# Optimization experiments

Measured on AMD Instinct MI355X. Metric: run time of the kernel, lower is better.

Reference implementation:

```python
import jax, jax.numpy as jnp
import numpy as np

G, K, C, H, D, L = 256, 88, 256, 8, 32, 4
NID, GATE, HID, ACT, NW = 16, 128, 256, 4644, 1
N = G * K
DEG = 16
E_RAND = N * DEG


def setup_inputs() -> dict:
    key = jax.random.key(0)
    ks = jax.random.split(key, 32)
    x = jax.random.normal(ks[0], (N, NID), dtype=jnp.float32)
    # within-graph random edges + self loops (PyG GATv2 add_self_loops=True)
    goff = jnp.repeat(jnp.arange(G, dtype=jnp.int64), K * DEG) * K
    src = goff + jax.random.randint(ks[1], (E_RAND,), 0, K, dtype=jnp.int64)
    dst = goff + jax.random.randint(ks[2], (E_RAND,), 0, K, dtype=jnp.int64)
    loops = jnp.arange(N, dtype=jnp.int64)
    edge_index = jnp.stack([jnp.concatenate([src, loops]), jnp.concatenate([dst, loops])])
    batch_map = jnp.repeat(jnp.arange(G, dtype=jnp.int64), K)

    def lin(k, fi, fo):
        return jax.random.normal(k, (fi, fo), dtype=jnp.float32) / np.sqrt(fi)

    inp = dict(x=x, edge_index=edge_index, batch_map=batch_map, num_graphs=G)
    inp['W_emb'] = lin(ks[3], NID, C); inp['b_emb'] = jnp.zeros((C,), jnp.float32)
    inp['pos_emb'] = jax.random.normal(ks[4], (K, C), dtype=jnp.float32)
    inp['gat_Wsrc'] = jax.random.normal(ks[5], (L, C, C), dtype=jnp.float32) / np.sqrt(C)
    inp['gat_Wdst'] = jax.random.normal(ks[6], (L, C, C), dtype=jnp.float32) / np.sqrt(C)
    inp['gat_att'] = jax.random.normal(ks[7], (L, H, D), dtype=jnp.float32) / np.sqrt(D)
    inp['gat_bias'] = jnp.zeros((L, C), jnp.float32)
    inp['ln_g'] = jnp.ones((L, C), jnp.float32); inp['ln_b'] = jnp.zeros((L, C), jnp.float32)
    inp['gW1'] = lin(ks[8], C, GATE); inp['gb1'] = jnp.zeros((GATE,), jnp.float32)
    inp['gW2'] = lin(ks[9], GATE, 1); inp['gb2'] = jnp.zeros((1,), jnp.float32)
    inp['pW1'] = lin(ks[10], C, HID); inp['pb1'] = jnp.zeros((HID,), jnp.float32)
    inp['p_ln_g'] = jnp.ones((HID,), jnp.float32); inp['p_ln_b'] = jnp.zeros((HID,), jnp.float32)
    inp['pW2'] = lin(ks[11], HID, ACT); inp['pb2'] = jnp.zeros((ACT,), jnp.float32)
    inp['vW1'] = lin(ks[12], C, HID); inp['vb1'] = jnp.zeros((HID,), jnp.float32)
    inp['vW2'] = lin(ks[13], HID, NW); inp['vb2'] = jnp.zeros((NW,), jnp.float32)
    return inp


def _layernorm(h, g, b):
    mu = h.mean(-1, keepdims=True)
    var = h.var(-1, keepdims=True)
    return (h - mu) * jax.lax.rsqrt(var + 1e-5) * g + b


def _segment_softmax(e, seg, num):
    m = jax.ops.segment_max(e, seg, num_segments=num)
    a = jnp.exp(e - m[seg])
    d = jax.ops.segment_sum(a, seg, num_segments=num)
    return a / d[seg]


def reference(x, edge_index, batch_map, num_graphs, W_emb, b_emb, pos_emb,
              gat_Wsrc, gat_Wdst, gat_att, gat_bias, ln_g, ln_b,
              gW1, gb1, gW2, gb2, pW1, pb1, p_ln_g, p_ln_b, pW2, pb2,
              vW1, vb1, vW2, vb2):
    n = x.shape[0]
    src, dst = edge_index[0], edge_index[1]
    h = jax.nn.relu(x @ W_emb + b_emb)
    positions = jnp.arange(n) % pos_emb.shape[0]  # arange(K) repeated per graph
    h = h + pos_emb[positions]
    for l in range(gat_Wsrc.shape[0]):
        xl = (h @ gat_Wsrc[l]).reshape(n, H, D)  # source transform
        xr = (h @ gat_Wdst[l]).reshape(n, H, D)  # target transform
        z = jax.nn.leaky_relu(xl[src] + xr[dst], negative_slope=0.2)  # [E,H,D]
        e = jnp.einsum('ehd,hd->eh', z, gat_att[l])
        alpha = _segment_softmax(e, dst, n)  # softmax over incoming edges
        out = jax.ops.segment_sum(alpha[:, :, None] * xl[src], dst, num_segments=n)
        out = out.reshape(n, -1) + gat_bias[l]
        h = _layernorm(h + jax.nn.relu(out), ln_g[l], ln_b[l])
    # gated attentional pooling over graphs
    gate = (jax.nn.relu(h @ gW1 + gb1) @ gW2 + gb2)[:, 0]
    a = _segment_softmax(gate, batch_map, num_graphs)
    emb = jax.ops.segment_sum(a[:, None] * h, batch_map, num_segments=num_graphs)
    policy = jax.nn.relu(_layernorm(emb @ pW1 + pb1, p_ln_g, p_ln_b)) @ pW2 + pb2
    value = jnp.tanh(jax.nn.relu(emb @ vW1 + vb1) @ vW2 + vb2)
    return policy, value
```

## Files before the change

### kernel.cpp

```cpp
#include <hip/hip_runtime.h>
#include <math.h>

constexpr int CN = 256;
constexpr int NHEAD = 8;
constexpr int KPG = 88;
constexpr int NIDF = 16;
constexpr int GATE_DIM = 128;
constexpr int ACT_DIM = 4644;
constexpr float LOG2E = 1.4426950408889634f;

typedef __attribute__((ext_vector_type(8))) short bf16x8;
typedef __attribute__((ext_vector_type(4))) float f32x4;

__device__ __forceinline__ unsigned short f2bf(float f) {
    unsigned int u = __float_as_uint(f);
    unsigned int r = (u + 0x7fffu + ((u >> 16) & 1u)) >> 16;
    return (unsigned short)r;
}
__device__ __forceinline__ float bf2f(unsigned short h) {
    return __uint_as_float(((unsigned int)h) << 16);
}

__device__ __forceinline__ void glds16(const void* g, void* l) {
    __builtin_amdgcn_global_load_lds(
        (const __attribute__((address_space(1))) unsigned int*)g,
        (__attribute__((address_space(3))) unsigned int*)l, 16, 0, 0);
}

__device__ __forceinline__ float fexp2(float x) {
    float r;
    asm("v_exp_f32 %0, %1" : "=v"(r) : "v"(x));
    return r;
}

__device__ __forceinline__ float grp8_sum(float p) {
    int t;
    t = __builtin_amdgcn_mov_dpp(__float_as_int(p), 0xB1, 0xF, 0xF, true);
    p += __int_as_float(t);
    t = __builtin_amdgcn_mov_dpp(__float_as_int(p), 0x4E, 0xF, 0xF, true);
    p += __int_as_float(t);
    t = __builtin_amdgcn_mov_dpp(__float_as_int(p), 0x141, 0xF, 0xF, true);
    p += __int_as_float(t);
    return p;
}

__global__ void count_kernel(const int* __restrict__ dst, int* __restrict__ cnt, int E) {
    int e = blockIdx.x * 256 + threadIdx.x;
    if (e < E) atomicAdd(&cnt[dst[e]], 1);
}

__global__ __launch_bounds__(1024) void scan1_kernel(const int* __restrict__ cnt,
                                                     int* __restrict__ rowptr,
                                                     int* __restrict__ btot, int n) {
    __shared__ int buf[1024];
    int tid = threadIdx.x;
    int i = blockIdx.x * 1024 + tid;
    int v = (i < n) ? cnt[i] : 0;
    buf[tid] = v;
    __syncthreads();
    for (int off = 1; off < 1024; off <<= 1) {
        int t = (tid >= off) ? buf[tid - off] : 0;
        __syncthreads();
        buf[tid] += t;
        __syncthreads();
    }
    if (i < n) rowptr[i] = buf[tid] - v;
    if (tid == 1023) btot[blockIdx.x] = buf[1023];
}

__global__ void scan2_kernel(int* __restrict__ btot, int nb) {
    if (threadIdx.x == 0 && blockIdx.x == 0) {
        int s = 0;
        for (int b = 0; b < nb; ++b) { int t = btot[b]; btot[b] = s; s += t; }
        btot[nb] = s;
    }
}

__global__ __launch_bounds__(1024) void scan3_kernel(int* __restrict__ rowptr,
                                                     const int* __restrict__ btot,
                                                     int n, int nb) {
    int i = blockIdx.x * 1024 + threadIdx.x;
    if (i < n) rowptr[i] += btot[i >> 10];
    else if (i == n) rowptr[n] = btot[nb];
}

__global__ void fill_kernel(const int* __restrict__ src, const int* __restrict__ dst,
                            const int* __restrict__ rowptr, int* __restrict__ cursor,
                            int* __restrict__ csrcB, int E) {
    int e = blockIdx.x * 256 + threadIdx.x;
    if (e < E) {
        int d = dst[e];
        int p = atomicAdd(&cursor[d], 1);
        csrcB[rowptr[d] + p] = src[e] * 1024;
    }
}

__global__ __launch_bounds__(256) void embed_kernel(const float* __restrict__ x,
                                                    const float* __restrict__ Wemb,
                                                    const float* __restrict__ bemb,
                                                    const float* __restrict__ pos,
                                                    float* __restrict__ h,
                                                    unsigned short* __restrict__ hh) {
    __shared__ float Wl[NIDF][CN];
    int tid = threadIdx.x;
    for (int i = tid; i < NIDF * CN; i += 256) Wl[i >> 8][i & 255] = Wemb[i];
    __syncthreads();
    float bias = bemb[tid];
    int node0 = blockIdx.x * 16;
    for (int q = 0; q < 16; ++q) {
        int n = node0 + q;
        float acc = bias;
        #pragma unroll
        for (int k = 0; k < NIDF; ++k) acc += x[n * NIDF + k] * Wl[k][tid];
        float val = fmaxf(acc, 0.f) + pos[(n % KPG) * CN + tid];
        h[(size_t)n * CN + tid] = val;
        hh[(size_t)n * CN + tid] = f2bf(val);
    }
}

__global__ void wconv_cat_kernel(const float* __restrict__ Ws, const float* __restrict__ Wd,
                                 unsigned short* __restrict__ Bh,
                                 unsigned short* __restrict__ Bl, int NB, int tot) {
    int o = blockIdx.x * 256 + threadIdx.x;
    if (o >= tot) return;
    int l4 = blockIdx.y;
    const float* ws = Ws + (size_t)l4 * 256 * 256;
    const float* wd = Wd + (size_t)l4 * 256 * 256;
    int idx = o & 511;
    int nb = (o >> 9) % NB;
    int kb = o / (512 * NB);
    int l = idx >> 3, j = idx & 7;
    int k = kb * 32 + (l >> 4) * 8 + j;
    int c = nb * 16 + (l & 15);
    float v = (c < 256) ? ws[(size_t)k * 256 + c] : wd[(size_t)k * 256 + (c - 256)];
    unsigned short hh = f2bf(v);
    Bh[(size_t)l4 * tot + o] = hh;
    Bl[(size_t)l4 * tot + o] = f2bf(v - bf2f(hh));
}

__global__ void wconv_kernel(const float* __restrict__ W, unsigned short* __restrict__ Bh,
                             unsigned short* __restrict__ Bl, int Nn, int NB, int tot) {
    int o = blockIdx.x * 256 + threadIdx.x;
    if (o >= tot) return;
    int idx = o & 511;
    int nb = (o >> 9) % NB;
    int kb = o / (512 * NB);
    int l = idx >> 3, j = idx & 7;
    int k = kb * 32 + (l >> 4) * 8 + j;
    int c = nb * 16 + (l & 15);
    float v = (c < Nn) ? W[(size_t)k * Nn + c] : 0.f;
    unsigned short hh = f2bf(v);
    Bh[o] = hh;
    Bl[o] = f2bf(v - bf2f(hh));
}

template <bool BIAS, bool THREE, bool OBF16, int NBT>
__global__ __launch_bounds__(256) void mgemm(const unsigned short* __restrict__ Ah,
                                             const unsigned short* __restrict__ Al,
                                             const unsigned short* __restrict__ Bh,
                                             const unsigned short* __restrict__ Bl,
                                             const float* __restrict__ bias,
                                             void* __restrict__ Cv,
                                             int M, int Nlog, int NB, int K) {
    constexpr int NF = NBT / 2;
    __shared__ unsigned short AhL[8 * 64 * 8];
    __shared__ unsigned short AlL[THREE ? 8 * 64 * 8 : 16];
    __shared__ unsigned short BhL[NBT * 512];
    __shared__ unsigned short BlL[NBT * 512];
    int tid = threadIdx.x;
    int wid = tid >> 6, lane = tid & 63;
    int row0 = blockIdx.x * 128;
    int cb = blockIdx.y;
    int wr = wid >> 1, wc = wid & 1;

    int rr = lane & 15, kq = lane >> 4;

    f32x4 acc[4][NF] = {};

    for (int k0 = 0; k0 < K; k0 += 32) {
        int kb = k0 >> 5;
        {
            int mb0 = wid * 2;
            const unsigned short* s0 = Ah + (size_t)(row0 + mb0 * 16 + rr) * K + k0 + kq * 8;
            const unsigned short* s1 = Ah + (size_t)(row0 + mb0 * 16 + 16 + rr) * K + k0 + kq * 8;
            glds16(s0, &AhL[mb0 * 512]);
            glds16(s1, &AhL[mb0 * 512 + 512]);
            if constexpr (THREE) {
                const unsigned short* t0 = Al + (size_t)(row0 + mb0 * 16 + rr) * K + k0 + kq * 8;
                const unsigned short* t1 = Al + (size_t)(row0 + mb0 * 16 + 16 + rr) * K + k0 + kq * 8;
                glds16(t0, &AlL[mb0 * 512]);
                glds16(t1, &AlL[mb0 * 512 + 512]);
            }
        }
        {
            size_t base = ((size_t)kb * NB + (size_t)cb * NBT) * 512;
            for (int ch = wid; ch < NBT; ch += 4) {
                glds16(Bh + base + ch * 512 + lane * 8, &BhL[ch * 512]);
                glds16(Bl + base + ch * 512 + lane * 8, &BlL[ch * 512]);
            }
        }
        __syncthreads();
        bf16x8 a_h[4], a_l[4], b_h[NF], b_l[NF];
        #pragma unroll
        for (int mf = 0; mf < 4; ++mf) {
            int off = ((wr * 4 + mf) * 64 + lane) * 8;
            a_h[mf] = *reinterpret_cast<const bf16x8*>(&AhL[off]);
            if constexpr (THREE)
                a_l[mf] = *reinterpret_cast<const bf16x8*>(&AlL[off]);
        }
        #pragma unroll
        for (int nf = 0; nf < NF; ++nf) {
            int off = ((wc * NF + nf) * 64 + lane) * 8;
            b_h[nf] = *reinterpret_cast<const bf16x8*>(&BhL[off]);
            b_l[nf] = *reinterpret_cast<const bf16x8*>(&BlL[off]);
        }
        #pragma unroll
        for (int mf = 0; mf < 4; ++mf)
            #pragma unroll
            for (int nf = 0; nf < NF; ++nf) {
                acc[mf][nf] = __builtin_amdgcn_mfma_f32_16x16x32_bf16(a_h[mf], b_h[nf], acc[mf][nf], 0, 0, 0);
                acc[mf][nf] = __builtin_amdgcn_mfma_f32_16x16x32_bf16(a_h[mf], b_l[nf], acc[mf][nf], 0, 0, 0);
                if constexpr (THREE)
                    acc[mf][nf] = __builtin_amdgcn_mfma_f32_16x16x32_bf16(a_l[mf], b_h[nf], acc[mf][nf], 0, 0, 0);
            }
        __syncthreads();
    }
    #pragma unroll
    for (int mf = 0; mf < 4; ++mf) {
        #pragma unroll
        for (int nf = 0; nf < NF; ++nf) {
            int col = cb * (NBT * 16) + wc * (NF * 16) + nf * 16 + (lane & 15);
            if (col < Nlog) {
                float bv = BIAS ? bias[col] : 0.f;
                #pragma unroll
                for (int rg = 0; rg < 4; ++rg) {
                    int row = row0 + wr * 64 + mf * 16 + (lane >> 4) * 4 + rg;
                    float r = acc[mf][nf][rg] + bv;
                    if constexpr (OBF16)
                        ((unsigned short*)Cv)[(size_t)row * Nlog + col] = f2bf(r);
                    else
                        ((float*)Cv)[(size_t)row * Nlog + col] = r;
                }
            }
        }
    }
}

__global__ __launch_bounds__(64) void gat_agg(const unsigned short* __restrict__ xlr,
                                              const int* __restrict__ rowptr,
                                              const int* __restrict__ csrcB,
                                              const float* __restrict__ att,
                                              const float* __restrict__ bias,
                                              const float* __restrict__ lng,
                                              const float* __restrict__ lnb,
                                              float* __restrict__ h,
                                              unsigned short* __restrict__ hh) {
    int cpx = gridDim.x >> 3;
    int swz = (blockIdx.x & 7) * cpx + (blockIdx.x >> 3);
    int lane = threadIdx.x;
    int n = __builtin_amdgcn_readfirstlane(swz);
    int voff = lane * 8;

    ushort4 ur = *reinterpret_cast<const ushort4*>(xlr + (size_t)n * 512 + 256 + lane * 4);
    float xr0 = bf2f(ur.x), xr1 = bf2f(ur.y), xr2 = bf2f(ur.z), xr3 = bf2f(ur.w);
    float4 at4 = *reinterpret_cast<const float4*>(att + lane * 4);
    at4.x *= LOG2E; at4.y *= LOG2E; at4.z *= LOG2E; at4.w *= LOG2E;
    float4 hr4 = *reinterpret_cast<const float4*>(h + (size_t)n * CN + lane * 4);

    int e0 = __builtin_amdgcn_readfirstlane(rowptr[n]);
    int e1 = __builtin_amdgcn_readfirstlane(rowptr[n + 1]);
    int last = e1 - 1;

    float s_r = 0.f;
    float a0 = 0.f, a1 = 0.f, a2 = 0.f, a3 = 0.f;
    const char* xB = (const char*)xlr;

    auto ld4 = [&](ushort4* X, int eb) {
        if (eb + 3 <= last) {
            #pragma unroll
            for (int j = 0; j < 4; ++j) {
                int f = csrcB[eb + j];
                X[j] = *reinterpret_cast<const ushort4*>(xB + (unsigned)f + voff);
            }
        } else {
            #pragma unroll
            for (int j = 0; j < 4; ++j) {
                int f = csrcB[min(eb + j, last)];
                X[j] = *reinterpret_cast<const ushort4*>(xB + (unsigned)f + voff);
            }
        }
    };
    auto group4 = [&](const ushort4* X, int eb) {
        float xf[4][4];
        #pragma unroll
        for (int j = 0; j < 4; ++j) {
            xf[j][0] = bf2f(X[j].x);
            xf[j][1] = bf2f(X[j].y);
            xf[j][2] = bf2f(X[j].z);
            xf[j][3] = bf2f(X[j].w);
        }
        float p[4];
        #pragma unroll
        for (int j = 0; j < 4; ++j) {
            float z, pp = 0.f;
            z = xf[j][0] + xr0; z = fmaxf(z, 0.2f * z); pp += z * at4.x;
            z = xf[j][1] + xr1; z = fmaxf(z, 0.2f * z); pp += z * at4.y;
            z = xf[j][2] + xr2; z = fmaxf(z, 0.2f * z); pp += z * at4.z;
            z = xf[j][3] + xr3; z = fmaxf(z, 0.2f * z); pp += z * at4.w;
            p[j] = grp8_sum(pp);
        }
        float w[4];
        if (eb + 3 < e1) {
            #pragma unroll
            for (int j = 0; j < 4; ++j) w[j] = fexp2(fminf(p[j], 80.f));
        } else {
            #pragma unroll
            for (int j = 0; j < 4; ++j) {
                float pc = (eb + j < e1) ? fminf(p[j], 80.f) : -INFINITY;
                w[j] = fexp2(pc);
            }
        }
        s_r += (w[0] + w[1]) + (w[2] + w[3]);
        #pragma unroll
        for (int j = 0; j < 4; ++j) {
            a0 += w[j] * xf[j][0];
            a1 += w[j] * xf[j][1];
            a2 += w[j] * xf[j][2];
            a3 += w[j] * xf[j][3];
        }
    };

    ushort4 A[4], B[4];
    ld4(A, e0);
    ld4(B, e0 + 4);
    for (int e = e0; e < e1; e += 8) {
        group4(A, e);
        if (e + 8 < e1) ld4(A, e + 8);
        if (e + 4 < e1) {
            group4(B, e + 4);
            if (e + 12 < e1) ld4(B, e + 12);
        }
    }

    float inv = 1.f / s_r;
    float4 bi4 = *reinterpret_cast<const float4*>(bias + lane * 4);
    float v0 = hr4.x + fmaxf(a0 * inv + bi4.x, 0.f);
    float v1 = hr4.y + fmaxf(a1 * inv + bi4.y, 0.f);
    float v2 = hr4.z + fmaxf(a2 * inv + bi4.z, 0.f);
    float v3 = hr4.w + fmaxf(a3 * inv + bi4.w, 0.f);

    float sum = v0 + v1 + v2 + v3;
    float sq = v0 * v0 + v1 * v1 + v2 * v2 + v3 * v3;
    #pragma unroll
    for (int o = 32; o; o >>= 1) { sum += __shfl_xor(sum, o); sq += __shfl_xor(sq, o); }
    float mu = sum / CN;
    float var = sq / CN - mu * mu;
    float ninv = rsqrtf(var + 1e-5f);
    float4 lg4 = *reinterpret_cast<const float4*>(lng + lane * 4);
    float4 lb4 = *reinterpret_cast<const float4*>(lnb + lane * 4);
    float o0 = (v0 - mu) * ninv * lg4.x + lb4.x;
    float o1 = (v1 - mu) * ninv * lg4.y + lb4.y;
    float o2 = (v2 - mu) * ninv * lg4.z + lb4.z;
    float o3 = (v3 - mu) * ninv * lg4.w + lb4.w;
    *reinterpret_cast<float4*>(h + (size_t)n * CN + lane * 4) = make_float4(o0, o1, o2, o3);

    ushort4 uh;
    uh.x = f2bf(o0); uh.y = f2bf(o1); uh.z = f2bf(o2); uh.w = f2bf(o3);
    *reinterpret_cast<ushort4*>(hh + (size_t)n * CN + lane * 4) = uh;
}

__global__ __launch_bounds__(256) void gate2_kernel(const float* __restrict__ gtmp,
                                                    const float* __restrict__ gW2,
                                                    const float* __restrict__ gb2,
                                                    float* __restrict__ gate, int N) {
    int n = blockIdx.x * 4 + (threadIdx.x >> 6);
    if (n >= N) return;
    int lane = threadIdx.x & 63;
    float2 t = *reinterpret_cast<const float2*>(gtmp + (size_t)n * GATE_DIM + lane * 2);
    float2 w = *reinterpret_cast<const float2*>(gW2 + lane * 2);
    float c = fmaxf(t.x, 0.f) * w.x + fmaxf(t.y, 0.f) * w.y;
    #pragma unroll
    for (int o = 32; o; o >>= 1) c += __shfl_xor(c, o);
    if (lane == 0) gate[n] = c + gb2[0];
}

__global__ __launch_bounds__(256) void pool_kernel(const float* __restrict__ gate,
                                                   const float* __restrict__ h,
                                                   float* __restrict__ emb) {
    __shared__ float a[KPG];
    __shared__ float wm[4];
    int g = blockIdx.x, tid = threadIdx.x;
    int wid = tid >> 6, lane = tid & 63;
    float gv = (tid < KPG) ? gate[g * KPG + tid] : -INFINITY;
    float m = gv;
    #pragma unroll
    for (int o = 32; o; o >>= 1) m = fmaxf(m, __shfl_xor(m, o));
    if (lane == 0) wm[wid] = m;
    __syncthreads();
    m = fmaxf(fmaxf(wm[0], wm[1]), fmaxf(wm[2], wm[3]));
    __syncthreads();
    float av = (tid < KPG) ? expf(gv - m) : 0.f;
    if (tid < KPG) a[tid] = av;
    float s = av;
    #pragma unroll
    for (int o = 32; o; o >>= 1) s += __shfl_xor(s, o);
    if (lane == 0) wm[wid] = s;
    __syncthreads();
    s = wm[0] + wm[1] + wm[2] + wm[3];
    float inv = 1.f / s;
    float acc = 0.f;
    const float* hg = h + (size_t)g * KPG * CN;
    for (int i = 0; i < KPG; ++i) acc += a[i] * hg[i * CN + tid];
    emb[(size_t)g * CN + tid] = acc * inv;
}

__global__ __launch_bounds__(256) void head_kernel(const float* __restrict__ emb,
    const float* __restrict__ pW1, const float* __restrict__ pb1,
    const float* __restrict__ plng, const float* __restrict__ plnb,
    const float* __restrict__ vW1, const float* __restrict__ vb1,
    const float* __restrict__ vW2, const float* __restrict__ vb2,
    unsigned short* __restrict__ t1h, unsigned short* __restrict__ t1l,
    float* __restrict__ value_out) {
    __shared__ float e_l[CN];
    __shared__ float rsum[4], rsq[4];
    int g = blockIdx.x, tid = threadIdx.x;
    int wid = tid >> 6, lane = tid & 63;
    e_l[tid] = emb[(size_t)g * CN + tid];
    __syncthreads();
    float p = pb1[tid], v = vb1[tid];
    for (int k = 0; k < CN; ++k) {
        float e = e_l[k];
        p += e * pW1[k * CN + tid];
        v += e * vW1[k * CN + tid];
    }
    float sum = p, sq = p * p;
    #pragma unroll
    for (int o = 32; o; o >>= 1) { sum += __shfl_xor(sum, o); sq += __shfl_xor(sq, o); }
    if (lane == 0) { rsum[wid] = sum; rsq[wid] = sq; }
    __syncthreads();
    sum = rsum[0] + rsum[1] + rsum[2] + rsum[3];
    sq  = rsq[0] + rsq[1] + rsq[2] + rsq[3];
    float mu = sum / CN;
    float var = sq / CN - mu * mu;
    float inv = rsqrtf(var + 1e-5f);
    float t1v = fmaxf((p - mu) * inv * plng[tid] + plnb[tid], 0.f);
    unsigned short th = f2bf(t1v);
    t1h[(size_t)g * CN + tid] = th;
    t1l[(size_t)g * CN + tid] = f2bf(t1v - bf2f(th));
    float contrib = fmaxf(v, 0.f) * vW2[tid];
    __syncthreads();
    #pragma unroll
    for (int o = 32; o; o >>= 1) contrib += __shfl_xor(contrib, o);
    if (lane == 0) rsum[wid] = contrib;
    __syncthreads();
    if (tid == 0)
        value_out[g] = tanhf(rsum[0] + rsum[1] + rsum[2] + rsum[3] + vb2[0]);
}

extern "C" void kernel_launch(void* const* d_in, const int* in_sizes, int n_in,
                              void* d_out, int out_size, void* d_ws, size_t ws_size,
                              hipStream_t stream) {
    const float* x        = (const float*)d_in[0];
    const int*   ei       = (const int*)d_in[1];
    const float* W_emb    = (const float*)d_in[4];
    const float* b_emb    = (const float*)d_in[5];
    const float* pos_emb  = (const float*)d_in[6];
    const float* gat_Wsrc = (const float*)d_in[7];
    const float* gat_Wdst = (const float*)d_in[8];
    const float* gat_att  = (const float*)d_in[9];
    const float* gat_bias = (const float*)d_in[10];
    const float* ln_g     = (const float*)d_in[11];
    const float* ln_b     = (const float*)d_in[12];
    const float* gW1      = (const float*)d_in[13];
    const float* gb1      = (const float*)d_in[14];
    const float* gW2      = (const float*)d_in[15];
    const float* gb2      = (const float*)d_in[16];
    const float* pW1      = (const float*)d_in[17];
    const float* pb1      = (const float*)d_in[18];
    const float* p_ln_g   = (const float*)d_in[19];
    const float* p_ln_b   = (const float*)d_in[20];
    const float* pW2      = (const float*)d_in[21];
    const float* pb2      = (const float*)d_in[22];
    const float* vW1      = (const float*)d_in[23];
    const float* vb1      = (const float*)d_in[24];
    const float* vW2      = (const float*)d_in[25];
    const float* vb2      = (const float*)d_in[26];

    const int N = in_sizes[2];
    const int E = in_sizes[1] / 2;
    const int G = N / KPG;
    const int NB_SC = (N + 1023) / 1024;

    const int NB_CAT = 32;
    const int NB_G1  = 8;
    const int GY_POL = (ACT_DIM + 63) / 64;
    const int NB_POL = GY_POL * 4;

    char* ws = (char*)d_ws;
    size_t off = 0;
    auto alloc = [&](size_t nbytes) {
        void* pp = ws + off;
        off = (off + nbytes + 255) & ~(size_t)255;
        return pp;
    };
    float* h      = (float*)alloc((size_t)N * CN * 4);
    unsigned short* hh = (unsigned short*)alloc((size_t)N * CN * 2);
    unsigned short* xlr = (unsigned short*)alloc((size_t)N * 512 * 2);
    float* gtmp   = (float*)alloc((size_t)N * GATE_DIM * 4);
    unsigned short* WcatH = (unsigned short*)alloc((size_t)4 * 8 * NB_CAT * 512 * 2);
    unsigned short* WcatL = (unsigned short*)alloc((size_t)4 * 8 * NB_CAT * 512 * 2);
    unsigned short* gW1H  = (unsigned short*)alloc((size_t)8 * NB_G1 * 512 * 2);
    unsigned short* gW1L  = (unsigned short*)alloc((size_t)8 * NB_G1 * 512 * 2);
    unsigned short* pW2H  = (unsigned short*)alloc((size_t)8 * NB_POL * 512 * 2);
    unsigned short* pW2L  = (unsigned short*)alloc((size_t)8 * NB_POL * 512 * 2);
    float* gate   = (float*)alloc((size_t)N * 4);
    float* emb    = (float*)alloc((size_t)G * CN * 4);
    unsigned short* t1h = (unsigned short*)alloc((size_t)G * CN * 2);
    unsigned short* t1l = (unsigned short*)alloc((size_t)G * CN * 2);
    int*   rowptr = (int*)alloc((size_t)(N + 1) * 4);
    int*   cnt    = (int*)alloc((size_t)N * 4);
    int*   cursor = (int*)alloc((size_t)N * 4);
    int*   btot   = (int*)alloc((size_t)64 * 4);
    int*   csrcB  = (int*)alloc((size_t)E * 4);

    const int* e_src = ei;
    const int* e_dst = ei + E;

    hipMemsetAsync(cnt, 0, (size_t)N * 4, stream);
    hipMemsetAsync(cursor, 0, (size_t)N * 4, stream);
    count_kernel<<<(E + 255) / 256, 256, 0, stream>>>(e_dst, cnt, E);
    scan1_kernel<<<NB_SC, 1024, 0, stream>>>(cnt, rowptr, btot, N);
    scan2_kernel<<<1, 64, 0, stream>>>(btot, NB_SC);
    scan3_kernel<<<(N + 1024) / 1024, 1024, 0, stream>>>(rowptr, btot, N, NB_SC);
    fill_kernel<<<(E + 255) / 256, 256, 0, stream>>>(e_src, e_dst, rowptr, cursor, csrcB, E);

    embed_kernel<<<N / 16, 256, 0, stream>>>(x, W_emb, b_emb, pos_emb, h, hh);

    {
        int totc = 8 * NB_CAT * 512;
        dim3 gw((totc + 255) / 256, 4);
        wconv_cat_kernel<<<gw, 256, 0, stream>>>(gat_Wsrc, gat_Wdst, WcatH, WcatL, NB_CAT, totc);
        int totg = 8 * NB_G1 * 512;
        wconv_kernel<<<(totg + 255) / 256, 256, 0, stream>>>(gW1, gW1H, gW1L, GATE_DIM, NB_G1, totg);
        int totp = 8 * NB_POL * 512;
        wconv_kernel<<<(totp + 255) / 256, 256, 0, stream>>>(pW2, pW2H, pW2L, ACT_DIM, NB_POL, totp);
    }

    for (int l = 0; l < 4; ++l) {
        size_t wo = (size_t)l * 8 * NB_CAT * 512;
        dim3 g1(N / 128, 512 / 128);
        mgemm<false, false, true, 8><<<g1, 256, 0, stream>>>(hh, nullptr, WcatH + wo, WcatL + wo,
                                                             nullptr, xlr, N, 512, NB_CAT, CN);
        gat_agg<<<N, 64, 0, stream>>>(xlr, rowptr, csrcB, gat_att + l * CN,
                                      gat_bias + l * CN, ln_g + l * CN, ln_b + l * CN,
                                      h, hh);
    }

    {
        dim3 g1(N / 128, 1);
        mgemm<true, false, false, 8><<<g1, 256, 0, stream>>>(hh, nullptr, gW1H, gW1L, gb1,
                                                             gtmp, N, GATE_DIM, NB_G1, CN);
        gate2_kernel<<<(N + 3) / 4, 256, 0, stream>>>(gtmp, gW2, gb2, gate, N);
    }
    pool_kernel<<<G, 256, 0, stream>>>(gate, h, emb);

    float* policy = (float*)d_out;
    float* value  = (float*)d_out + (size_t)G * ACT_DIM;
    head_kernel<<<G, 256, 0, stream>>>(emb, pW1, pb1, p_ln_g, p_ln_b,
                                       vW1, vb1, vW2, vb2, t1h, t1l, value);
    dim3 g2(G / 128, GY_POL);
    mgemm<true, true, false, 4><<<g2, 256, 0, stream>>>(t1h, t1l, pW2H, pW2L, pb2,
                                                        policy, G, ACT_DIM, NB_POL, CN);
}
```

Baseline: 304.1 us.

## Drop weight low-bf16 term in GAT GEMMs; process two nodes per aggregation wave

The mgemm template takes a product count, so the per-layer GAT projection and the gate GEMM use only the high bf16 part of the weights (one MFMA instead of two, with no Bl loads or LDS). The gat_agg kernel now handles two destination nodes per 64-thread block and interleaves their edge-gather loops, which gives more memory-level parallelism and halves the block count. The cost is lower precision in the weight products and more register pressure in the aggregation kernel.

```diff
diff --git a/kernel.cpp b/kernel.cpp
--- a/kernel.cpp
+++ b/kernel.cpp
@@ -154,7 +154,7 @@
     Bl[o] = f2bf(v - bf2f(hh));
 }
 
-template <bool BIAS, bool THREE, bool OBF16, int NBT>
+template <bool BIAS, int PROD, bool OBF16, int NBT>
 __global__ __launch_bounds__(256) void mgemm(const unsigned short* __restrict__ Ah,
                                              const unsigned short* __restrict__ Al,
                                              const unsigned short* __restrict__ Bh,
@@ -164,9 +164,9 @@
                                              int M, int Nlog, int NB, int K) {
     constexpr int NF = NBT / 2;
     __shared__ unsigned short AhL[8 * 64 * 8];
-    __shared__ unsigned short AlL[THREE ? 8 * 64 * 8 : 16];
+    __shared__ unsigned short AlL[(PROD >= 3) ? 8 * 64 * 8 : 16];
     __shared__ unsigned short BhL[NBT * 512];
-    __shared__ unsigned short BlL[NBT * 512];
+    __shared__ unsigned short BlL[(PROD >= 2) ? NBT * 512 : 16];
     int tid = threadIdx.x;
     int wid = tid >> 6, lane = tid & 63;
     int row0 = blockIdx.x * 128;
@@ -185,7 +185,7 @@
             const unsigned short* s1 = Ah + (size_t)(row0 + mb0 * 16 + 16 + rr) * K + k0 + kq * 8;
             glds16(s0, &AhL[mb0 * 512]);
             glds16(s1, &AhL[mb0 * 512 + 512]);
-            if constexpr (THREE) {
+            if constexpr (PROD >= 3) {
                 const unsigned short* t0 = Al + (size_t)(row0 + mb0 * 16 + rr) * K + k0 + kq * 8;
                 const unsigned short* t1 = Al + (size_t)(row0 + mb0 * 16 + 16 + rr) * K + k0 + kq * 8;
                 glds16(t0, &AlL[mb0 * 512]);
@@ -196,7 +196,8 @@
             size_t base = ((size_t)kb * NB + (size_t)cb * NBT) * 512;
             for (int ch = wid; ch < NBT; ch += 4) {
                 glds16(Bh + base + ch * 512 + lane * 8, &BhL[ch * 512]);
-                glds16(Bl + base + ch * 512 + lane * 8, &BlL[ch * 512]);
+                if constexpr (PROD >= 2)
+                    glds16(Bl + base + ch * 512 + lane * 8, &BlL[ch * 512]);
             }
         }
         __syncthreads();
@@ -205,22 +206,24 @@
         for (int mf = 0; mf < 4; ++mf) {
             int off = ((wr * 4 + mf) * 64 + lane) * 8;
             a_h[mf] = *reinterpret_cast<const bf16x8*>(&AhL[off]);
-            if constexpr (THREE)
+            if constexpr (PROD >= 3)
                 a_l[mf] = *reinterpret_cast<const bf16x8*>(&AlL[off]);
         }
         #pragma unroll
         for (int nf = 0; nf < NF; ++nf) {
             int off = ((wc * NF + nf) * 64 + lane) * 8;
             b_h[nf] = *reinterpret_cast<const bf16x8*>(&BhL[off]);
-            b_l[nf] = *reinterpret_cast<const bf16x8*>(&BlL[off]);
+            if constexpr (PROD >= 2)
+                b_l[nf] = *reinterpret_cast<const bf16x8*>(&BlL[off]);
         }
         #pragma unroll
         for (int mf = 0; mf < 4; ++mf)
             #pragma unroll
             for (int nf = 0; nf < NF; ++nf) {
                 acc[mf][nf] = __builtin_amdgcn_mfma_f32_16x16x32_bf16(a_h[mf], b_h[nf], acc[mf][nf], 0, 0, 0);
-                acc[mf][nf] = __builtin_amdgcn_mfma_f32_16x16x32_bf16(a_h[mf], b_l[nf], acc[mf][nf], 0, 0, 0);
-                if constexpr (THREE)
+                if constexpr (PROD >= 2)
+                    acc[mf][nf] = __builtin_amdgcn_mfma_f32_16x16x32_bf16(a_h[mf], b_l[nf], acc[mf][nf], 0, 0, 0);
+                if constexpr (PROD >= 3)
                     acc[mf][nf] = __builtin_amdgcn_mfma_f32_16x16x32_bf16(a_l[mf], b_h[nf], acc[mf][nf], 0, 0, 0);
             }
         __syncthreads();
@@ -258,24 +261,27 @@
     int cpx = gridDim.x >> 3;
     int swz = (blockIdx.x & 7) * cpx + (blockIdx.x >> 3);
     int lane = threadIdx.x;
-    int n = __builtin_amdgcn_readfirstlane(swz);
+    int na = __builtin_amdgcn_readfirstlane(swz * 2);
+    int nb_ = na + 1;
     int voff = lane * 8;
 
-    ushort4 ur = *reinterpret_cast<const ushort4*>(xlr + (size_t)n * 512 + 256 + lane * 4);
-    float xr0 = bf2f(ur.x), xr1 = bf2f(ur.y), xr2 = bf2f(ur.z), xr3 = bf2f(ur.w);
+    ushort4 ua = *reinterpret_cast<const ushort4*>(xlr + (size_t)na * 512 + 256 + lane * 4);
+    ushort4 ub = *reinterpret_cast<const ushort4*>(xlr + (size_t)nb_ * 512 + 256 + lane * 4);
+    float xa0 = bf2f(ua.x), xa1 = bf2f(ua.y), xa2 = bf2f(ua.z), xa3 = bf2f(ua.w);
+    float xb0 = bf2f(ub.x), xb1 = bf2f(ub.y), xb2 = bf2f(ub.z), xb3 = bf2f(ub.w);
     float4 at4 = *reinterpret_cast<const float4*>(att + lane * 4);
     at4.x *= LOG2E; at4.y *= LOG2E; at4.z *= LOG2E; at4.w *= LOG2E;
-    float4 hr4 = *reinterpret_cast<const float4*>(h + (size_t)n * CN + lane * 4);
-
-    int e0 = __builtin_amdgcn_readfirstlane(rowptr[n]);
-    int e1 = __builtin_amdgcn_readfirstlane(rowptr[n + 1]);
-    int last = e1 - 1;
-
-    float s_r = 0.f;
-    float a0 = 0.f, a1 = 0.f, a2 = 0.f, a3 = 0.f;
+
+    int e0a = __builtin_amdgcn_readfirstlane(rowptr[na]);
+    int e1a = __builtin_amdgcn_readfirstlane(rowptr[na + 1]);
+    int e1b = __builtin_amdgcn_readfirstlane(rowptr[nb_ + 1]);
+    int e0b = e1a;
+
+    float sA = 0.f, aA0 = 0.f, aA1 = 0.f, aA2 = 0.f, aA3 = 0.f;
+    float sB = 0.f, aB0 = 0.f, aB1 = 0.f, aB2 = 0.f, aB3 = 0.f;
     const char* xB = (const char*)xlr;
 
-    auto ld4 = [&](ushort4* X, int eb) {
+    auto ld4 = [&](ushort4* X, int eb, int last) {
         if (eb + 3 <= last) {
             #pragma unroll
             for (int j = 0; j < 4; ++j) {
@@ -290,7 +296,9 @@
             }
         }
     };
-    auto group4 = [&](const ushort4* X, int eb) {
+    auto group4 = [&](const ushort4* X, int eb, int e1,
+                      float xr0, float xr1, float xr2, float xr3,
+                      float& s_r, float& a0, float& a1, float& a2, float& a3) {
         float xf[4][4];
         #pragma unroll
         for (int j = 0; j < 4; ++j) {
@@ -330,43 +338,55 @@
         }
     };
 
-    ushort4 A[4], B[4];
-    ld4(A, e0);
-    ld4(B, e0 + 4);
-    for (int e = e0; e < e1; e += 8) {
-        group4(A, e);
-        if (e + 8 < e1) ld4(A, e + 8);
-        if (e + 4 < e1) {
-            group4(B, e + 4);
-            if (e + 12 < e1) ld4(B, e + 12);
-        }
-    }
-
-    float inv = 1.f / s_r;
-    float4 bi4 = *reinterpret_cast<const float4*>(bias + lane * 4);
-    float v0 = hr4.x + fmaxf(a0 * inv + bi4.x, 0.f);
-    float v1 = hr4.y + fmaxf(a1 * inv + bi4.y, 0.f);
-    float v2 = hr4.z + fmaxf(a2 * inv + bi4.z, 0.f);
-    float v3 = hr4.w + fmaxf(a3 * inv + bi4.w, 0.f);
-
-    float sum = v0 + v1 + v2 + v3;
-    float sq = v0 * v0 + v1 * v1 + v2 * v2 + v3 * v3;
-    #pragma unroll
-    for (int o = 32; o; o >>= 1) { sum += __shfl_xor(sum, o); sq += __shfl_xor(sq, o); }
-    float mu = sum / CN;
-    float var = sq / CN - mu * mu;
-    float ninv = rsqrtf(var + 1e-5f);
-    float4 lg4 = *reinterpret_cast<const float4*>(lng + lane * 4);
-    float4 lb4 = *reinterpret_cast<const float4*>(lnb + lane * 4);
-    float o0 = (v0 - mu) * ninv * lg4.x + lb4.x;
-    float o1 = (v1 - mu) * ninv * lg4.y + lb4.y;
-    float o2 = (v2 - mu) * ninv * lg4.z + lb4.z;
-    float o3 = (v3 - mu) * ninv * lg4.w + lb4.w;
-    *reinterpret_cast<float4*>(h + (size_t)n * CN + lane * 4) = make_float4(o0, o1, o2, o3);
-
-    ushort4 uh;
-    uh.x = f2bf(o0); uh.y = f2bf(o1); uh.z = f2bf(o2); uh.w = f2bf(o3);
-    *reinterpret_cast<ushort4*>(hh + (size_t)n * CN + lane * 4) = uh;
+    ushort4 A[4], B[4], T[4];
+    int eA = e0a, eB = e0b;
+    ld4(A, eA, e1a - 1);
+    ld4(B, eB, e1b - 1);
+    while (eA < e1a || eB < e1b) {
+        if (eA < e1a) {
+            #pragma unroll
+            for (int j = 0; j < 4; ++j) T[j] = A[j];
+            if (eA + 4 < e1a) ld4(A, eA + 4, e1a - 1);
+            group4(T, eA, e1a, xa0, xa1, xa2, xa3, sA, aA0, aA1, aA2, aA3);
+            eA += 4;
+        }
+        if (eB < e1b) {
+            #pragma unroll
+            for (int j = 0; j < 4; ++j) T[j] = B[j];
+            if (eB + 4 < e1b) ld4(B, eB + 4, e1b - 1);
+            group4(T, eB, e1b, xb0, xb1, xb2, xb3, sB, aB0, aB1, aB2, aB3);
+            eB += 4;
+        }
+    }
+
+    auto finish = [&](int n, float s_r, float a0, float a1, float a2, float a3) {
+        float inv = 1.f / s_r;
+        float4 hr4 = *reinterpret_cast<const float4*>(h + (size_t)n * CN + lane * 4);
+        float4 bi4 = *reinterpret_cast<const float4*>(bias + lane * 4);
+        float v0 = hr4.x + fmaxf(a0 * inv + bi4.x, 0.f);
+        float v1 = hr4.y + fmaxf(a1 * inv + bi4.y, 0.f);
+        float v2 = hr4.z + fmaxf(a2 * inv + bi4.z, 0.f);
+        float v3 = hr4.w + fmaxf(a3 * inv + bi4.w, 0.f);
+        float sum = v0 + v1 + v2 + v3;
+        float sq = v0 * v0 + v1 * v1 + v2 * v2 + v3 * v3;
+        #pragma unroll
+        for (int o = 32; o; o >>= 1) { sum += __shfl_xor(sum, o); sq += __shfl_xor(sq, o); }
+        float mu = sum / CN;
+        float var = sq / CN - mu * mu;
+        float ninv = rsqrtf(var + 1e-5f);
+        float4 lg4 = *reinterpret_cast<const float4*>(lng + lane * 4);
+        float4 lb4 = *reinterpret_cast<const float4*>(lnb + lane * 4);
+        float o0 = (v0 - mu) * ninv * lg4.x + lb4.x;
+        float o1 = (v1 - mu) * ninv * lg4.y + lb4.y;
+        float o2 = (v2 - mu) * ninv * lg4.z + lb4.z;
+        float o3 = (v3 - mu) * ninv * lg4.w + lb4.w;
+        *reinterpret_cast<float4*>(h + (size_t)n * CN + lane * 4) = make_float4(o0, o1, o2, o3);
+        ushort4 uh;
+        uh.x = f2bf(o0); uh.y = f2bf(o1); uh.z = f2bf(o2); uh.w = f2bf(o3);
+        *reinterpret_cast<ushort4*>(hh + (size_t)n * CN + lane * 4) = uh;
+    };
+    finish(na, sA, aA0, aA1, aA2, aA3);
+    finish(nb_, sB, aB0, aB1, aB2, aB3);
 }
 
 __global__ __launch_bounds__(256) void gate2_kernel(const float* __restrict__ gtmp,
@@ -549,17 +569,17 @@
     for (int l = 0; l < 4; ++l) {
         size_t wo = (size_t)l * 8 * NB_CAT * 512;
         dim3 g1(N / 128, 512 / 128);
-        mgemm<false, false, true, 8><<<g1, 256, 0, stream>>>(hh, nullptr, WcatH + wo, WcatL + wo,
-                                                             nullptr, xlr, N, 512, NB_CAT, CN);
-        gat_agg<<<N, 64, 0, stream>>>(xlr, rowptr, csrcB, gat_att + l * CN,
-                                      gat_bias + l * CN, ln_g + l * CN, ln_b + l * CN,
-                                      h, hh);
+        mgemm<false, 1, true, 8><<<g1, 256, 0, stream>>>(hh, nullptr, WcatH + wo, WcatL + wo,
+                                                         nullptr, xlr, N, 512, NB_CAT, CN);
+        gat_agg<<<N / 2, 64, 0, stream>>>(xlr, rowptr, csrcB, gat_att + l * CN,
+                                          gat_bias + l * CN, ln_g + l * CN, ln_b + l * CN,
+                                          h, hh);
     }
 
     {
         dim3 g1(N / 128, 1);
-        mgemm<true, false, false, 8><<<g1, 256, 0, stream>>>(hh, nullptr, gW1H, gW1L, gb1,
-                                                             gtmp, N, GATE_DIM, NB_G1, CN);
+        mgemm<true, 1, false, 8><<<g1, 256, 0, stream>>>(hh, nullptr, gW1H, gW1L, gb1,
+                                                         gtmp, N, GATE_DIM, NB_G1, CN);
         gate2_kernel<<<(N + 3) / 4, 256, 0, stream>>>(gtmp, gW2, gb2, gate, N);
     }
     pool_kernel<<<G, 256, 0, stream>>>(gate, h, emb);
@@ -569,6 +589,6 @@
     head_kernel<<<G, 256, 0, stream>>>(emb, pW1, pb1, p_ln_g, p_ln_b,
                                        vW1, vb1, vW2, vb2, t1h, t1l, value);
     dim3 g2(G / 128, GY_POL);
-    mgemm<true, true, false, 4><<<g2, 256, 0, stream>>>(t1h, t1l, pW2H, pW2L, pb2,
-                                                        policy, G, ACT_DIM, NB_POL, CN);
-}
+    mgemm<true, 3, false, 4><<<g2, 256, 0, stream>>>(t1h, t1l, pW2H, pW2L, pb2,
+                                                     policy, G, ACT_DIM, NB_POL, CN);
+}
```

New measurement: 289.7 us. 4.8% less time.
